# Kernel optimization log

Measured on AMD Instinct MI355X. Metric: run time of the kernel, lower is better.

Reference implementation:

```python
import jax, jax.numpy as jnp
import numpy as np

B, N, F_IN, H, L, C = 64, 512, 21, 64, 3, 9
NEG_INF = -jnp.inf


def setup_inputs() -> dict:
    key = jax.random.key(0)
    ks = jax.random.split(key, 24)
    s = lambda shape, k, scale=0.05: jax.random.normal(ks[k], shape, dtype=jnp.float32) * scale
    return {
        "node_features": jax.random.normal(ks[0], (B, N, F_IN), dtype=jnp.float32),
        "adjacency": jax.random.bernoulli(ks[1], 0.05, (B, N, N)).astype(jnp.float32),
        "node_mask": jnp.ones((B, N), dtype=bool),
        "We": s((F_IN, H), 2), "be": jnp.zeros((H,), jnp.float32),
        "Wl": s((L, H, H), 3), "a_src": s((L, H), 4), "a_dst": s((L, H), 5),
        "gamma": jnp.ones((L, H), jnp.float32), "beta": jnp.zeros((L, H), jnp.float32),
        "P1": s((H, H), 6), "pb1": jnp.zeros((H,), jnp.float32),
        "P2": s((H,), 7), "pb2": jnp.zeros((), jnp.float32),
        "C1": s((H, H), 8), "cb1": jnp.zeros((H,), jnp.float32),
        "C2": s((H, C), 9), "cb2": jnp.zeros((C,), jnp.float32),
    }


def _layernorm(x, g, b, eps=1e-5):
    mu = x.mean(-1, keepdims=True)
    var = ((x - mu) ** 2).mean(-1, keepdims=True)
    return (x - mu) * jax.lax.rsqrt(var + eps) * g + b


def reference(node_features, adjacency, node_mask, We, be, Wl, a_src, a_dst,
              gamma, beta, P1, pb1, P2, pb2, C1, cb1, C2, cb2):
    # node embedding (dropout = identity in eval)
    h = jax.nn.relu(node_features @ We + be)  # [B,N,H]
    adj_zero = adjacency == 0
    for l in range(L):
        hW = h @ Wl[l]                                  # [B,N,H]
        attn = hW @ a_src[l]                            # [B,N] src scores
        attn = attn[:, :, None] + (hW @ a_dst[l])[:, None, :]  # [B,N,N]
        attn = jax.nn.leaky_relu(attn, 0.2)
        attn = jnp.where(adj_zero, NEG_INF, attn)
        attn = jnp.nan_to_num(jax.nn.softmax(attn, axis=-1), nan=0.0)
        h = _layernorm(h + attn @ hW, gamma[l], beta[l])
    # attention pooling
    pa = jnp.tanh(h @ P1 + pb1) @ P2 + pb2              # [B,N]
    pa = jnp.where(node_mask, pa, NEG_INF)
    pa = jnp.nan_to_num(jax.nn.softmax(pa, axis=-1), nan=0.0)
    g = jnp.einsum('bn,bnh->bh', pa, h)                 # [B,H]
    return jax.nn.relu(g @ C1 + cb1) @ C2 + cb2         # [B,C]
```

## Files before the change

kernel.cpp:

```cpp
#include <hip/hip_runtime.h>


#define WS_H     0
#define WS_HWA   2097152
#define WS_HWB   4194304
#define WS_SA    6291456
#define WS_TA    6324224
#define WS_SB    6356992
#define WS_TB    6389760
#define WS_PA    6422528
#define WS_DEG   6455296
#define WS_LIST_BYTES 25952256

typedef const __attribute__((address_space(1))) unsigned int gu32;
typedef __attribute__((address_space(3))) unsigned int lu32;

__device__ __forceinline__ void gl_lds16(const float* g, float* l) {
  __builtin_amdgcn_global_load_lds((gu32*)g, (lu32*)l, 16, 0, 0);
}

template <int CTRL>
__device__ __forceinline__ float dpp_add(float v) {
  int x = __builtin_amdgcn_update_dpp(0, __float_as_int(v), CTRL, 0xf, 0xf, true);
  return v + __int_as_float(x);
}
__device__ __forceinline__ float wtot(float v) {
  v = dpp_add<0x111>(v);
  v = dpp_add<0x112>(v);
  v = dpp_add<0x114>(v);
  v = dpp_add<0x118>(v);
  v = dpp_add<0x142>(v);
  v = dpp_add<0x143>(v);
  return __int_as_float(__builtin_amdgcn_readlane(__float_as_int(v), 63));
}
__device__ __forceinline__ float rsum16d(float v) {
  v = dpp_add<0x111>(v);
  v = dpp_add<0x112>(v);
  v = dpp_add<0x114>(v);
  v = dpp_add<0x118>(v);
  return v;
}

__device__ __forceinline__ float wsum(float v) {
#pragma unroll
  for (int o = 32; o; o >>= 1) v += __shfl_xor(v, o, 64);
  return v;
}
__device__ __forceinline__ float wmax(float v) {
#pragma unroll
  for (int o = 32; o; o >>= 1) v = fmaxf(v, __shfl_xor(v, o, 64));
  return v;
}

__global__ __launch_bounds__(512) void k_embed_hw(
    const float* __restrict__ x, const float* __restrict__ We,
    const float* __restrict__ be, const float* __restrict__ adj,
    const float* __restrict__ W0, const float* __restrict__ asrc,
    const float* __restrict__ adst,
    float* __restrict__ h, int* __restrict__ deg,
    unsigned short* __restrict__ nlist,
    float* __restrict__ hW, float* __restrict__ s, float* __restrict__ t) {
  __shared__ float lw[64 * 68];
  __shared__ float lhT[64 * 34];
  __shared__ unsigned short lidx[8][4][64];
  int tid = threadIdx.x, lane = tid & 63, wv = tid >> 6;
  int blk = blockIdx.x;
  int xcd = blk & 7, i = blk >> 3;
  int b = xcd * 8 + (i & 7), sub = i >> 3;
  int base = b * 512 + sub * 32;
  int rb = base + wv * 4;
#pragma unroll
  for (int k = 0; k < 2; ++k) {
    int idx = tid + 512 * k;
    int rr = idx >> 4, q = idx & 15;
    *(float4*)&lw[rr * 68 + q * 4] = *(const float4*)&W0[rr * 64 + q * 4];
  }
  float wreg[21];
#pragma unroll
  for (int f = 0; f < 21; ++f) wreg[f] = We[f * 64 + lane];
  float bev = be[lane];
  unsigned long long lmask = (1ull << lane) - 1ull;
  float4 a0[4], a1[4];
#pragma unroll
  for (int r = 0; r < 4; ++r) {
    const float4* ar = (const float4*)(adj + (size_t)(rb + r) * 512);
    a0[r] = ar[lane];
    a1[r] = ar[64 + lane];
  }
#pragma unroll
  for (int r = 0; r < 4; ++r) {
    int row = rb + r;
    const float* xr = x + (size_t)row * 21;
    float acc = bev;
#pragma unroll
    for (int f = 0; f < 21; ++f) acc = fmaf(xr[f], wreg[f], acc);
    acc = fmaxf(acc, 0.0f);
    h[(size_t)row * 64 + lane] = acc;
    lhT[lane * 34 + (wv * 4 + r)] = acc;
    float comp[8] = {a0[r].x, a0[r].y, a0[r].z, a0[r].w,
                     a1[r].x, a1[r].y, a1[r].z, a1[r].w};
    int cnt = 0;
#pragma unroll
    for (int c = 0; c < 8; ++c) {
      bool on = comp[c] != 0.0f;
      unsigned long long m = __ballot(on);
      if (on) {
        int pos = cnt + __popcll(m & lmask);
        int col = (c < 4) ? (lane * 4 + c) : (256 + lane * 4 + (c - 4));
        if (pos < 64) lidx[wv][r][pos] = (unsigned short)col;
      }
      cnt += __popcll(m);
    }
    if (lane == 0) deg[row] = cnt < 64 ? cnt : 64;
  }
  {
    ushort4 v = *(ushort4*)&lidx[wv][0][lane * 4];
    *(ushort4*)(nlist + (size_t)rb * 64 + lane * 4) = v;
  }
  __syncthreads();
  if (tid < 128) {
    int tc = tid & 15, tr = tid >> 4;
    float acc[4][4] = {};
#pragma unroll 4
    for (int c = 0; c < 64; ++c) {
      float2 a01 = *(const float2*)&lhT[c * 34 + tr * 4];
      float2 a23 = *(const float2*)&lhT[c * 34 + tr * 4 + 2];
      float4 bb = *(const float4*)&lw[c * 68 + tc * 4];
      float av[4] = {a01.x, a01.y, a23.x, a23.y};
      float bv[4] = {bb.x, bb.y, bb.z, bb.w};
#pragma unroll
      for (int ii = 0; ii < 4; ++ii)
#pragma unroll
        for (int j = 0; j < 4; ++j)
          acc[ii][j] = fmaf(av[ii], bv[j], acc[ii][j]);
    }
    float p1[4], p2[4];
#pragma unroll
    for (int j = 0; j < 4; ++j) {
      p1[j] = asrc[tc * 4 + j];
      p2[j] = adst[tc * 4 + j];
    }
#pragma unroll
    for (int ii = 0; ii < 4; ++ii) {
      int row = base + tr * 4 + ii;
      *(float4*)&hW[(size_t)row * 64 + tc * 4] =
          make_float4(acc[ii][0], acc[ii][1], acc[ii][2], acc[ii][3]);
      float ps = acc[ii][0] * p1[0] + acc[ii][1] * p1[1] +
                 acc[ii][2] * p1[2] + acc[ii][3] * p1[3];
      float pt = acc[ii][0] * p2[0] + acc[ii][1] * p2[1] +
                 acc[ii][2] * p2[2] + acc[ii][3] * p2[3];
      ps = rsum16d(ps);
      pt = rsum16d(pt);
      if (tc == 15) { s[row] = ps; t[row] = pt; }
    }
  }
}

template <int MODE>
__global__ __launch_bounds__(1024) void k_layer(
    float* __restrict__ h, const float* __restrict__ hWin,
    const float* __restrict__ sIn, const float* __restrict__ tIn,
    const int* __restrict__ deg, const unsigned short* __restrict__ nlist,
    const float* __restrict__ gamma, const float* __restrict__ beta,
    const float* __restrict__ Wn, const float* __restrict__ v1,
    const float* __restrict__ v2,
    float* __restrict__ hWout, float* __restrict__ sOut,
    float* __restrict__ tOut) {
  __shared__ float hlds[512 * 64];
  __shared__ float lw[64 * 68];
  __shared__ float tlds[512];
  int tid = threadIdx.x, lane = tid & 63, wv = tid >> 6;
  int blk = blockIdx.x;
  int b = (blk & 7) * 8 + ((blk >> 3) & 7);
  int sub = blk >> 6;
  int base = b * 512 + sub * 128;
  int rb = base + wv * 8;

  unsigned short jr[8]; float sir[8], hrr[8]; int dgr[8];
#pragma unroll
  for (int r = 0; r < 8; ++r) {
    int row = rb + r;
    jr[r] = nlist[(size_t)row * 64 + lane];
    sir[r] = sIn[row];
    hrr[r] = h[(size_t)row * 64 + lane];
    dgr[r] = deg[row];
  }
  {
    int rr = tid >> 4, q = tid & 15;
    *(float4*)&lw[rr * 68 + q * 4] = *(const float4*)&Wn[rr * 64 + q * 4];
  }
  const float* tb = tIn + ((size_t)b << 9);
  if (tid < 128) *(float4*)&tlds[tid * 4] = *(const float4*)&tb[tid * 4];
  {
    const char* src = (const char*)(hWin + ((size_t)b << 9) * 64);
    char* dst = (char*)hlds;
#pragma unroll
    for (int c = 0; c < 8; ++c) {
      int off = wv * 8192 + c * 1024;
      gl_lds16((const float*)(src + off + lane * 16), (float*)(dst + off));
    }
  }
  __syncthreads();

  float gm = gamma[lane], bt = beta[lane];
  float hst[8];
#pragma unroll
  for (int rp = 0; rp < 8; rp += 2) {
    int dgA = __builtin_amdgcn_readfirstlane(dgr[rp]);
    int dgB = __builtin_amdgcn_readfirstlane(dgr[rp + 1]);
    bool actA = lane < dgA, actB = lane < dgB;
    int jmA = actA ? (int)jr[rp] : 0;
    int jmB = actB ? (int)jr[rp + 1] : 0;
    float eA = sir[rp] + (actA ? tlds[jmA] : 0.0f);
    float eB = sir[rp + 1] + (actB ? tlds[jmB] : 0.0f);
    eA = eA > 0.0f ? eA : 0.2f * eA;
    eB = eB > 0.0f ? eB : 0.2f * eB;
    float wjA = actA ? __expf(eA) : 0.0f;
    float wjB = actB ? __expf(eB) : 0.0f;
    int bitsA = __float_as_int(wjA) & ~511;
    int bitsB = __float_as_int(wjB) & ~511;
    int pkA = bitsA | jmA, pkB = bitsB | jmB;
    float a0A = 0.0f, a1A = 0.0f, a0B = 0.0f, a1B = 0.0f;
    int mA = (dgA + 7) & ~7, mB = (dgB + 7) & ~7;
    int mx = mA > mB ? mA : mB;
    for (int n = 0; n < mx; n += 8) {
      if (n < mA) {
#pragma unroll
        for (int k = 0; k < 8; k += 2) {
          int u0 = __builtin_amdgcn_readlane(pkA, n + k);
          int u1 = __builtin_amdgcn_readlane(pkA, n + k + 1);
          a0A = fmaf(__int_as_float(u0 & ~511),
                     hlds[(u0 & 511) * 64 + lane], a0A);
          a1A = fmaf(__int_as_float(u1 & ~511),
                     hlds[(u1 & 511) * 64 + lane], a1A);
        }
      }
      if (n < mB) {
#pragma unroll
        for (int k = 0; k < 8; k += 2) {
          int u0 = __builtin_amdgcn_readlane(pkB, n + k);
          int u1 = __builtin_amdgcn_readlane(pkB, n + k + 1);
          a0B = fmaf(__int_as_float(u0 & ~511),
                     hlds[(u0 & 511) * 64 + lane], a0B);
          a1B = fmaf(__int_as_float(u1 & ~511),
                     hlds[(u1 & 511) * 64 + lane], a1B);
        }
      }
    }
    float dsumA = wtot(__int_as_float(bitsA));
    float dsumB = wtot(__int_as_float(bitsB));
    float aA = dgA > 0 ? (a0A + a1A) * (1.0f / dsumA) : 0.0f;
    float aB = dgB > 0 ? (a0B + a1B) * (1.0f / dsumB) : 0.0f;
    float xvA = hrr[rp] + aA, xvB = hrr[rp + 1] + aB;
    float s1A = wtot(xvA), s2A = wtot(xvA * xvA);
    float s1B = wtot(xvB), s2B = wtot(xvB * xvB);
    float muA = s1A * 0.015625f, muB = s1B * 0.015625f;
    float varA = fmaf(-muA, muA, s2A * 0.015625f);
    float varB = fmaf(-muB, muB, s2B * 0.015625f);
    float hnA = fmaf((xvA - muA) * rsqrtf(varA + 1e-5f), gm, bt);
    float hnB = fmaf((xvB - muB) * rsqrtf(varB + 1e-5f), gm, bt);
    h[(size_t)(rb + rp) * 64 + lane] = hnA;
    h[(size_t)(rb + rp + 1) * 64 + lane] = hnB;
    hst[rp] = hnA;
    hst[rp + 1] = hnB;
  }
  __syncthreads();
  float* lhT = hlds;
#pragma unroll
  for (int r = 0; r < 8; ++r) lhT[lane * 132 + (wv * 8 + r)] = hst[r];
  __syncthreads();
  if (tid < 512) {
    int tc = tid & 15, tr = tid >> 4;
    float acc[4][4] = {};
#pragma unroll 4
    for (int c = 0; c < 64; ++c) {
      float4 aa = *(const float4*)&lhT[c * 132 + tr * 4];
      float4 bb = *(const float4*)&lw[c * 68 + tc * 4];
      float av[4] = {aa.x, aa.y, aa.z, aa.w};
      float bv[4] = {bb.x, bb.y, bb.z, bb.w};
#pragma unroll
      for (int ii = 0; ii < 4; ++ii)
#pragma unroll
        for (int j = 0; j < 4; ++j)
          acc[ii][j] = fmaf(av[ii], bv[j], acc[ii][j]);
    }
    float p1[4], p2[4];
#pragma unroll
    for (int j = 0; j < 4; ++j) { p1[j] = v1[tc * 4 + j]; p2[j] = v2[tc * 4 + j]; }
#pragma unroll
    for (int ii = 0; ii < 4; ++ii) {
      int row = base + tr * 4 + ii;
      if (MODE == 0) {
        *(float4*)&hWout[(size_t)row * 64 + tc * 4] =
            make_float4(acc[ii][0], acc[ii][1], acc[ii][2], acc[ii][3]);
        float ps = acc[ii][0] * p1[0] + acc[ii][1] * p1[1] +
                   acc[ii][2] * p1[2] + acc[ii][3] * p1[3];
        float pt = acc[ii][0] * p2[0] + acc[ii][1] * p2[1] +
                   acc[ii][2] * p2[2] + acc[ii][3] * p2[3];
        ps = rsum16d(ps);
        pt = rsum16d(pt);
        if (tc == 15) { sOut[row] = ps; tOut[row] = pt; }
      } else {
        float p = 0.0f;
#pragma unroll
        for (int j = 0; j < 4; ++j) p += tanhf(acc[ii][j] + p1[j]) * p2[j];
        p = rsum16d(p);
        if (tc == 15) sOut[row] = p;
      }
    }
  }
}

__global__ __launch_bounds__(512) void k_pool(const float* __restrict__ h,
    const float* __restrict__ pa, const float* __restrict__ C1,
    const float* __restrict__ cb1, const float* __restrict__ C2,
    const float* __restrict__ cb2, float* __restrict__ out) {
  __shared__ float red[8];
  __shared__ float gpart[8][64];
  __shared__ float gl[64], rl[64];
  int b = ((blockIdx.x & 7) << 3) | (blockIdx.x >> 3);
  int tid = threadIdx.x, lane = tid & 63, wv = tid >> 6;
  float v = pa[b * 512 + tid];
  float m = wmax(v);
  if (lane == 0) red[wv] = m;
  __syncthreads();
  float bm = red[0];
#pragma unroll
  for (int w = 1; w < 8; ++w) bm = fmaxf(bm, red[w]);
  float e = __expf(v - bm);
  float sm = wsum(e);
  __syncthreads();
  if (lane == 0) red[wv] = sm;
  __syncthreads();
  float bs = 0.0f;
#pragma unroll
  for (int w = 0; w < 8; ++w) bs += red[w];
  float p = e / bs;
  const float* hb = h + ((size_t)b * 512) * 64;
  float g = 0.0f;
#pragma unroll
  for (int l = 0; l < 64; ++l) {
    float pj = __shfl(p, l, 64);
    g = fmaf(pj, hb[(size_t)(wv * 64 + l) * 64 + lane], g);
  }
  gpart[wv][lane] = g;
  __syncthreads();
  if (wv == 0) {
    float gg = 0.0f;
#pragma unroll
    for (int w = 0; w < 8; ++w) gg += gpart[w][lane];
    gl[lane] = gg;
    float rr = cb1[lane];
#pragma unroll
    for (int j = 0; j < 64; ++j) rr = fmaf(gl[j], C1[j * 64 + lane], rr);
    rr = fmaxf(rr, 0.0f);
    rl[lane] = rr;
    if (lane < 9) {
      float o = cb2[lane];
#pragma unroll
      for (int k = 0; k < 64; ++k) o = fmaf(rl[k], C2[k * 9 + lane], o);
      out[b * 9 + lane] = o;
    }
  }
}

extern "C" void kernel_launch(void* const* d_in, const int* in_sizes, int n_in,
                              void* d_out, int out_size, void* d_ws, size_t ws_size,
                              hipStream_t stream) {
  const float* x    = (const float*)d_in[0];
  const float* adj  = (const float*)d_in[1];
  const float* We   = (const float*)d_in[3];
  const float* be   = (const float*)d_in[4];
  const float* Wl   = (const float*)d_in[5];
  const float* asrc = (const float*)d_in[6];
  const float* adst = (const float*)d_in[7];
  const float* gamma= (const float*)d_in[8];
  const float* beta = (const float*)d_in[9];
  const float* P1   = (const float*)d_in[10];
  const float* pb1  = (const float*)d_in[11];
  const float* P2   = (const float*)d_in[12];
  const float* C1   = (const float*)d_in[14];
  const float* cb1  = (const float*)d_in[15];
  const float* C2   = (const float*)d_in[16];
  const float* cb2  = (const float*)d_in[17];
  float* out = (float*)d_out;

  float* ws  = (float*)d_ws;
  float* h   = ws + WS_H;
  float* hwA = ws + WS_HWA;
  float* hwB = ws + WS_HWB;
  float* sA  = ws + WS_SA;
  float* tA  = ws + WS_TA;
  float* sB  = ws + WS_SB;
  float* tB  = ws + WS_TB;
  float* pa  = ws + WS_PA;
  int*   deg = (int*)(ws + WS_DEG);
  unsigned short* nlist = (unsigned short*)((char*)d_ws + WS_LIST_BYTES);

  k_embed_hw<<<1024, 512, 0, stream>>>(x, We, be, adj, Wl, asrc, adst,
                                       h, deg, nlist, hwA, sA, tA);
  k_layer<0><<<256, 1024, 0, stream>>>(h, hwA, sA, tA, deg, nlist,
                                       gamma, beta, Wl + 4096,
                                       asrc + 64, adst + 64, hwB, sB, tB);
  k_layer<0><<<256, 1024, 0, stream>>>(h, hwB, sB, tB, deg, nlist,
                                       gamma + 64, beta + 64, Wl + 8192,
                                       asrc + 128, adst + 128, hwA, sA, tA);
  k_layer<1><<<256, 1024, 0, stream>>>(h, hwA, sA, tA, deg, nlist,
                                       gamma + 128, beta + 128, P1, pb1, P2,
                                       nullptr, pa, nullptr);
  k_pool<<<64, 512, 0, stream>>>(h, pa, C1, cb1, C2, cb2, out);
}
```

Before: 218.9 us.

## Split wavefront halves across row pairs with float2 neighbor gathers

The sparse attention aggregation now processes two rows per wavefront at once. Each 32-lane half owns one row and each lane handles two feature columns, gathered as float2 LDS reads. This removes the serialized per-row neighbor loops and halves the number of LDS gather instructions. In exchange, the layernorm sums become 32-lane reductions with a per-half broadcast, and the loop runs to the larger of the two degrees, so work is wasted when the two degrees differ.

```diff
diff --git a/kernel.cpp b/kernel.cpp
--- a/kernel.cpp
+++ b/kernel.cpp
@@ -33,12 +33,23 @@
   v = dpp_add<0x143>(v);
   return __int_as_float(__builtin_amdgcn_readlane(__float_as_int(v), 63));
 }
+__device__ __forceinline__ float hsum32(float v) {
+  v = dpp_add<0x111>(v);
+  v = dpp_add<0x112>(v);
+  v = dpp_add<0x114>(v);
+  v = dpp_add<0x118>(v);
+  v = dpp_add<0x142>(v);
+  return v;
+}
 __device__ __forceinline__ float rsum16d(float v) {
   v = dpp_add<0x111>(v);
   v = dpp_add<0x112>(v);
   v = dpp_add<0x114>(v);
   v = dpp_add<0x118>(v);
   return v;
+}
+__device__ __forceinline__ float bcastf(float v, int l) {
+  return __int_as_float(__builtin_amdgcn_readlane(__float_as_int(v), l));
 }
 
 __device__ __forceinline__ float wsum(float v) {
@@ -170,21 +181,25 @@
   __shared__ float lw[64 * 68];
   __shared__ float tlds[512];
   int tid = threadIdx.x, lane = tid & 63, wv = tid >> 6;
+  int hl = lane & 31, half = lane >> 5;
   int blk = blockIdx.x;
   int b = (blk & 7) * 8 + ((blk >> 3) & 7);
   int sub = blk >> 6;
   int base = b * 512 + sub * 128;
   int rb = base + wv * 8;
 
-  unsigned short jr[8]; float sir[8], hrr[8]; int dgr[8];
+  unsigned short jr[8]; float sir[8]; int dgr[8];
+  float2 hr2[4];
 #pragma unroll
   for (int r = 0; r < 8; ++r) {
     int row = rb + r;
     jr[r] = nlist[(size_t)row * 64 + lane];
     sir[r] = sIn[row];
-    hrr[r] = h[(size_t)row * 64 + lane];
     dgr[r] = deg[row];
   }
+#pragma unroll
+  for (int p = 0; p < 4; ++p)
+    hr2[p] = *(const float2*)&h[(size_t)(rb + 2 * p + half) * 64 + hl * 2];
   {
     int rr = tid >> 4, q = tid & 15;
     *(float4*)&lw[rr * 68 + q * 4] = *(const float4*)&Wn[rr * 64 + q * 4];
@@ -202,17 +217,18 @@
   }
   __syncthreads();
 
-  float gm = gamma[lane], bt = beta[lane];
-  float hst[8];
-#pragma unroll
-  for (int rp = 0; rp < 8; rp += 2) {
-    int dgA = __builtin_amdgcn_readfirstlane(dgr[rp]);
-    int dgB = __builtin_amdgcn_readfirstlane(dgr[rp + 1]);
+  float2 gm2 = *(const float2*)&gamma[hl * 2];
+  float2 bt2 = *(const float2*)&beta[hl * 2];
+  float hn0s[4], hn1s[4];
+#pragma unroll
+  for (int p = 0; p < 4; ++p) {
+    int dgA = __builtin_amdgcn_readfirstlane(dgr[2 * p]);
+    int dgB = __builtin_amdgcn_readfirstlane(dgr[2 * p + 1]);
     bool actA = lane < dgA, actB = lane < dgB;
-    int jmA = actA ? (int)jr[rp] : 0;
-    int jmB = actB ? (int)jr[rp + 1] : 0;
-    float eA = sir[rp] + (actA ? tlds[jmA] : 0.0f);
-    float eB = sir[rp + 1] + (actB ? tlds[jmB] : 0.0f);
+    int jmA = actA ? (int)jr[2 * p] : 0;
+    int jmB = actB ? (int)jr[2 * p + 1] : 0;
+    float eA = sir[2 * p] + (actA ? tlds[jmA] : 0.0f);
+    float eB = sir[2 * p + 1] + (actB ? tlds[jmB] : 0.0f);
     eA = eA > 0.0f ? eA : 0.2f * eA;
     eB = eB > 0.0f ? eB : 0.2f * eB;
     float wjA = actA ? __expf(eA) : 0.0f;
@@ -220,54 +236,58 @@
     int bitsA = __float_as_int(wjA) & ~511;
     int bitsB = __float_as_int(wjB) & ~511;
     int pkA = bitsA | jmA, pkB = bitsB | jmB;
-    float a0A = 0.0f, a1A = 0.0f, a0B = 0.0f, a1B = 0.0f;
-    int mA = (dgA + 7) & ~7, mB = (dgB + 7) & ~7;
-    int mx = mA > mB ? mA : mB;
-    for (int n = 0; n < mx; n += 8) {
-      if (n < mA) {
-#pragma unroll
-        for (int k = 0; k < 8; k += 2) {
-          int u0 = __builtin_amdgcn_readlane(pkA, n + k);
-          int u1 = __builtin_amdgcn_readlane(pkA, n + k + 1);
-          a0A = fmaf(__int_as_float(u0 & ~511),
-                     hlds[(u0 & 511) * 64 + lane], a0A);
-          a1A = fmaf(__int_as_float(u1 & ~511),
-                     hlds[(u1 & 511) * 64 + lane], a1A);
-        }
+    float a0 = 0.0f, a1 = 0.0f, a2 = 0.0f, a3 = 0.0f;
+    int mx = dgA > dgB ? dgA : dgB;
+    int mx4 = (mx + 3) & ~3;
+    int hoff = hl * 2;
+    for (int n = 0; n < mx4; n += 4) {
+#pragma unroll
+      for (int k = 0; k < 4; k += 2) {
+        int uA0 = __builtin_amdgcn_readlane(pkA, n + k);
+        int uB0 = __builtin_amdgcn_readlane(pkB, n + k);
+        int uA1 = __builtin_amdgcn_readlane(pkA, n + k + 1);
+        int uB1 = __builtin_amdgcn_readlane(pkB, n + k + 1);
+        int u0 = half ? uB0 : uA0;
+        int u1 = half ? uB1 : uA1;
+        float2 d0 = *(const float2*)&hlds[(u0 & 511) * 64 + hoff];
+        float2 d1 = *(const float2*)&hlds[(u1 & 511) * 64 + hoff];
+        float w0 = __int_as_float(u0 & ~511);
+        float w1 = __int_as_float(u1 & ~511);
+        a0 = fmaf(w0, d0.x, a0);
+        a1 = fmaf(w0, d0.y, a1);
+        a2 = fmaf(w1, d1.x, a2);
+        a3 = fmaf(w1, d1.y, a3);
       }
-      if (n < mB) {
-#pragma unroll
-        for (int k = 0; k < 8; k += 2) {
-          int u0 = __builtin_amdgcn_readlane(pkB, n + k);
-          int u1 = __builtin_amdgcn_readlane(pkB, n + k + 1);
-          a0B = fmaf(__int_as_float(u0 & ~511),
-                     hlds[(u0 & 511) * 64 + lane], a0B);
-          a1B = fmaf(__int_as_float(u1 & ~511),
-                     hlds[(u1 & 511) * 64 + lane], a1B);
-        }
-      }
-    }
-    float dsumA = wtot(__int_as_float(bitsA));
-    float dsumB = wtot(__int_as_float(bitsB));
-    float aA = dgA > 0 ? (a0A + a1A) * (1.0f / dsumA) : 0.0f;
-    float aB = dgB > 0 ? (a0B + a1B) * (1.0f / dsumB) : 0.0f;
-    float xvA = hrr[rp] + aA, xvB = hrr[rp + 1] + aB;
-    float s1A = wtot(xvA), s2A = wtot(xvA * xvA);
-    float s1B = wtot(xvB), s2B = wtot(xvB * xvB);
-    float muA = s1A * 0.015625f, muB = s1B * 0.015625f;
-    float varA = fmaf(-muA, muA, s2A * 0.015625f);
-    float varB = fmaf(-muB, muB, s2B * 0.015625f);
-    float hnA = fmaf((xvA - muA) * rsqrtf(varA + 1e-5f), gm, bt);
-    float hnB = fmaf((xvB - muB) * rsqrtf(varB + 1e-5f), gm, bt);
-    h[(size_t)(rb + rp) * 64 + lane] = hnA;
-    h[(size_t)(rb + rp + 1) * 64 + lane] = hnB;
-    hst[rp] = hnA;
-    hst[rp + 1] = hnB;
+    }
+    float dsA = wtot(__int_as_float(bitsA));
+    float dsB = wtot(__int_as_float(bitsB));
+    float ds = half ? dsB : dsA;
+    int dgh = half ? dgB : dgA;
+    float inv = dgh > 0 ? __frcp_rn(ds) : 0.0f;
+    float av0 = (a0 + a2) * inv, av1 = (a1 + a3) * inv;
+    float xv0 = hr2[p].x + av0, xv1 = hr2[p].y + av1;
+    float s1h = hsum32(xv0 + xv1);
+    float s2h = hsum32(fmaf(xv0, xv0, xv1 * xv1));
+    float S1 = half ? bcastf(s1h, 63) : bcastf(s1h, 31);
+    float S2 = half ? bcastf(s2h, 63) : bcastf(s2h, 31);
+    float mu = S1 * 0.015625f;
+    float var = fmaf(-mu, mu, S2 * 0.015625f);
+    float rsq = rsqrtf(var + 1e-5f);
+    float hn0 = fmaf((xv0 - mu) * rsq, gm2.x, bt2.x);
+    float hn1 = fmaf((xv1 - mu) * rsq, gm2.y, bt2.y);
+    *(float2*)&h[(size_t)(rb + 2 * p + half) * 64 + hoff] =
+        make_float2(hn0, hn1);
+    hn0s[p] = hn0;
+    hn1s[p] = hn1;
   }
   __syncthreads();
   float* lhT = hlds;
 #pragma unroll
-  for (int r = 0; r < 8; ++r) lhT[lane * 132 + (wv * 8 + r)] = hst[r];
+  for (int p = 0; p < 4; ++p) {
+    int rr = wv * 8 + 2 * p + half;
+    lhT[(hl * 2) * 132 + rr] = hn0s[p];
+    lhT[(hl * 2 + 1) * 132 + rr] = hn1s[p];
+  }
   __syncthreads();
   if (tid < 512) {
     int tc = tid & 15, tr = tid >> 4;
```

Result: slower. 224.9 us (+2.7%).
